# Kernel optimization log

Measured on AMD Instinct MI355X. Metric: run time of the kernel, lower is better.

## Reference

```python
import jax, jax.numpy as jnp
import numpy as np

LN_EPS = 1e-5


def sage_conv(x_src, h_dst, src, dst, num_dst, W_self, W_neigh, b):
    # DGL SAGEConv, aggregator_type='mean':
    #   h_neigh[i] = mean_{(j->i) in E} x_src[j]
    #   out = h_dst @ W_self^T + h_neigh @ W_neigh^T + b
    msg = x_src[src]  # [E, F] neighbor gather (irregular access)
    agg = jax.ops.segment_sum(msg, dst, num_segments=num_dst)  # [num_dst, F]
    deg = jax.ops.segment_sum(jnp.ones((src.shape[0],), x_src.dtype), dst,
                              num_segments=num_dst)
    h_neigh = agg / jnp.maximum(deg, 1.0)[:, None]
    return h_dst @ W_self.T + h_neigh @ W_neigh.T + b


def setup_inputs() -> dict:
    key = jax.random.key(0)
    ks = jax.random.split(key, 12)
    N0, N1, N2 = 100000, 20000, 4000
    E1, E2 = 400000, 80000
    F_IN, F_H, F_OUT = 128, 256, 64
    x = jax.random.normal(ks[0], (N0, F_IN), dtype=jnp.float32)
    # layer-1 MFG edges (src -> dst); dst nodes are the prefix x[:N1]
    src1 = jax.random.randint(ks[1], (E1,), 0, N0)
    dst1 = jax.random.randint(ks[2], (E1,), 0, N1)
    # layer-2 MFG edges over the N1 layer-1 outputs
    src2 = jax.random.randint(ks[3], (E2,), 0, N1)
    dst2 = jax.random.randint(ks[4], (E2,), 0, N2)
    s_in = 1.0 / np.sqrt(F_IN)
    s_h = 1.0 / np.sqrt(F_H)
    W_self1 = jax.random.uniform(ks[5], (F_H, F_IN), jnp.float32, -s_in, s_in)
    W_neigh1 = jax.random.uniform(ks[6], (F_H, F_IN), jnp.float32, -s_in, s_in)
    b1 = jnp.zeros((F_H,), jnp.float32)
    W_self2 = jax.random.uniform(ks[7], (F_OUT, F_H), jnp.float32, -s_h, s_h)
    W_neigh2 = jax.random.uniform(ks[8], (F_OUT, F_H), jnp.float32, -s_h, s_h)
    b2 = jnp.zeros((F_OUT,), jnp.float32)
    return {"x": x, "W_self1": W_self1, "W_neigh1": W_neigh1, "b1": b1,
            "W_self2": W_self2, "W_neigh2": W_neigh2, "b2": b2,
            "src1": src1, "dst1": dst1, "src2": src2, "dst2": dst2,
            "num_dst1": N1, "num_dst2": N2, "num_bits": 0, "num_grad_bits": 0}


def reference(x, W_self1, W_neigh1, b1, W_self2, W_neigh2, b2,
              src1, dst1, src2, dst2, num_dst1, num_dst2,
              num_bits, num_grad_bits):
    # num_bits / num_grad_bits == 0 -> full precision (quantization is identity)
    h_dst = x[:num_dst1]
    h = sage_conv(x, h_dst, src1, dst1, num_dst1, W_self1, W_neigh1, b1)
    h = jax.nn.relu(h)
    # F.layer_norm(h, h.shape): normalize over the ENTIRE tensor, no affine
    mu = jnp.mean(h)
    var = jnp.mean(jnp.square(h - mu))
    h = (h - mu) / jnp.sqrt(var + LN_EPS)
    # dropout in eval mode: identity (deterministic reference)
    h2_dst = h[:num_dst2]
    return sage_conv(h, h2_dst, src2, dst2, num_dst2, W_self2, W_neigh2, b2)
```

## Files before the change

kernel.cpp:

```cpp
#include <hip/hip_runtime.h>

#define LN_EPS 1e-5f
#define CAP 128

typedef __attribute__((ext_vector_type(8))) short short8v;
typedef __attribute__((ext_vector_type(4))) float f32x4;

__device__ __forceinline__ unsigned short f2bf(float f) {
  union { float f; unsigned u; } v; v.f = f;
  unsigned r = v.u + 0x7FFFu + ((v.u >> 16) & 1u);
  return (unsigned short)(r >> 16);
}
__device__ __forceinline__ float bf2f(unsigned short b) {
  union { unsigned u; float f; } v; v.u = ((unsigned)b) << 16;
  return v.f;
}
__device__ __forceinline__ float lo16(unsigned v) { return bf2f((unsigned short)(v & 0xffff)); }
__device__ __forceinline__ float hi16(unsigned v) { return bf2f((unsigned short)(v >> 16)); }
__device__ __forceinline__ unsigned pack2(float lo, float hi) {
  return ((unsigned)f2bf(hi) << 16) | (unsigned)f2bf(lo);
}


__global__ __launch_bounds__(256) void k_prep(
    int* __restrict__ cntz, int nz4,
    const float* __restrict__ x, unsigned short* __restrict__ xbf, int n4x,
    const float* __restrict__ wa, unsigned short* __restrict__ oa, int na4,
    const float* __restrict__ wb, unsigned short* __restrict__ ob, int nb4,
    const float* __restrict__ wc, unsigned short* __restrict__ oc, int nc4,
    const float* __restrict__ wd, unsigned short* __restrict__ od, int nd4) {
  int i = blockIdx.x * 256 + threadIdx.x;
  if (i < nz4) { ((int4*)cntz)[i] = make_int4(0, 0, 0, 0); return; }
  i -= nz4;
  const float* src;
  unsigned short* dst;
  if (i < n4x) { src = x; dst = xbf; }
  else {
    i -= n4x;
    if (i < na4) { src = wa; dst = oa; }
    else { i -= na4;
      if (i < nb4) { src = wb; dst = ob; }
      else { i -= nb4;
        if (i < nc4) { src = wc; dst = oc; }
        else { i -= nc4;
          if (i < nd4) { src = wd; dst = od; }
          else return;
        }
      }
    }
  }
  float4 v = ((const float4*)src)[i];
  ushort4 o;
  o.x = f2bf(v.x); o.y = f2bf(v.y); o.z = f2bf(v.z); o.w = f2bf(v.w);
  ((ushort4*)dst)[i] = o;
}


__global__ void k_fill2(const int* __restrict__ s1, const int* __restrict__ d1, int E1,
                        int* __restrict__ c1, int* __restrict__ l1,
                        const int* __restrict__ s2, const int* __restrict__ d2, int E2,
                        int* __restrict__ c2, int* __restrict__ l2) {
  int e = blockIdx.x * blockDim.x + threadIdx.x;
  if (e < E1) {
    int d = d1[e];
    int p = atomicAdd(&c1[d], 1);
    if (p < CAP) l1[(size_t)d * CAP + p] = s1[e];
  } else if (e < E1 + E2) {
    int k = e - E1;
    int d = d2[k];
    int p = atomicAdd(&c2[d], 1);
    if (p < CAP) l2[(size_t)d * CAP + p] = s2[k];
  }
}


__global__ __launch_bounds__(256) void k_gather1(
    const unsigned short* __restrict__ X, const int* __restrict__ cnt,
    const int* __restrict__ sl, unsigned short* __restrict__ out, int nNodes) {
  constexpr int F = 128;
  const int d = blockIdx.x * 4 + (threadIdx.x >> 6);
  if (d >= nNodes) return;
  const int lane = threadIdx.x & 63;
  const int deg = min(cnt[d], CAP);
  const int b = d * CAP;
  float a0 = 0.f, a1 = 0.f;
  const unsigned short* Xl = X + lane * 2;

  for (int j = 0; j < deg; j += 64) {
    int idx = (j + lane < deg) ? sl[b + j + lane] : 0;
    const int n = min(64, deg - j);
    int t = 0;
    for (; t + 8 <= n; t += 8) {
      unsigned v0 = *(const unsigned*)(Xl + (size_t)__shfl(idx, t + 0) * F);
      unsigned v1 = *(const unsigned*)(Xl + (size_t)__shfl(idx, t + 1) * F);
      unsigned v2 = *(const unsigned*)(Xl + (size_t)__shfl(idx, t + 2) * F);
      unsigned v3 = *(const unsigned*)(Xl + (size_t)__shfl(idx, t + 3) * F);
      unsigned v4 = *(const unsigned*)(Xl + (size_t)__shfl(idx, t + 4) * F);
      unsigned v5 = *(const unsigned*)(Xl + (size_t)__shfl(idx, t + 5) * F);
      unsigned v6 = *(const unsigned*)(Xl + (size_t)__shfl(idx, t + 6) * F);
      unsigned v7 = *(const unsigned*)(Xl + (size_t)__shfl(idx, t + 7) * F);
      a0 += lo16(v0) + lo16(v1) + lo16(v2) + lo16(v3) +
            lo16(v4) + lo16(v5) + lo16(v6) + lo16(v7);
      a1 += hi16(v0) + hi16(v1) + hi16(v2) + hi16(v3) +
            hi16(v4) + hi16(v5) + hi16(v6) + hi16(v7);
    }
    for (; t < n; ++t) {
      unsigned v = *(const unsigned*)(Xl + (size_t)__shfl(idx, t) * F);
      a0 += lo16(v);
      a1 += hi16(v);
    }
  }

  const float sc = 1.f / fmaxf((float)deg, 1.f);
  *(unsigned*)(out + (size_t)d * F + lane * 2) = pack2(a0 * sc, a1 * sc);
}


__global__ __launch_bounds__(256) void k_gather2_fin(
    const unsigned short* __restrict__ X, const int* __restrict__ cnt,
    const int* __restrict__ sl, unsigned short* __restrict__ out, int nNodes, int nGB,
    const float* __restrict__ p1, const float* __restrict__ p2, int nPart,
    float* __restrict__ stats, float invN) {
  if ((int)blockIdx.x == nGB) {
    const int tid = threadIdx.x;
    float s1 = 0.f, s2 = 0.f;
    for (int i = tid; i < nPart; i += 256) { s1 += p1[i]; s2 += p2[i]; }
#pragma unroll
    for (int o = 32; o > 0; o >>= 1) {
      s1 += __shfl_down(s1, o);
      s2 += __shfl_down(s2, o);
    }
    __shared__ float l1[4], l2[4];
    if ((tid & 63) == 0) { l1[tid >> 6] = s1; l2[tid >> 6] = s2; }
    __syncthreads();
    if (tid == 0) {
      float t1 = l1[0] + l1[1] + l1[2] + l1[3];
      float t2 = l2[0] + l2[1] + l2[2] + l2[3];
      float mu = t1 * invN;
      float var = t2 * invN - mu * mu;
      stats[2] = mu;
      stats[3] = 1.f / sqrtf(var + LN_EPS);
    }
    return;
  }

  constexpr int F = 256;
  const int d = blockIdx.x * 4 + (threadIdx.x >> 6);
  if (d >= nNodes) return;
  const int lane = threadIdx.x & 63;
  const int deg = min(cnt[d], CAP);
  const int b = d * CAP;
  float a0 = 0.f, a1 = 0.f, a2 = 0.f, a3 = 0.f;
  const unsigned short* Xl = X + lane * 4;

  for (int j = 0; j < deg; j += 64) {
    int idx = (j + lane < deg) ? sl[b + j + lane] : 0;
    const int n = min(64, deg - j);
    int t = 0;
    for (; t + 4 <= n; t += 4) {
      uint2 v0 = *(const uint2*)(Xl + (size_t)__shfl(idx, t + 0) * F);
      uint2 v1 = *(const uint2*)(Xl + (size_t)__shfl(idx, t + 1) * F);
      uint2 v2 = *(const uint2*)(Xl + (size_t)__shfl(idx, t + 2) * F);
      uint2 v3 = *(const uint2*)(Xl + (size_t)__shfl(idx, t + 3) * F);
      a0 += lo16(v0.x) + lo16(v1.x) + lo16(v2.x) + lo16(v3.x);
      a1 += hi16(v0.x) + hi16(v1.x) + hi16(v2.x) + hi16(v3.x);
      a2 += lo16(v0.y) + lo16(v1.y) + lo16(v2.y) + lo16(v3.y);
      a3 += hi16(v0.y) + hi16(v1.y) + hi16(v2.y) + hi16(v3.y);
    }
    for (; t < n; ++t) {
      uint2 v = *(const uint2*)(Xl + (size_t)__shfl(idx, t) * F);
      a0 += lo16(v.x);
      a1 += hi16(v.x);
      a2 += lo16(v.y);
      a3 += hi16(v.y);
    }
  }

  const float sc = 1.f / fmaxf((float)deg, 1.f);
  uint2 v;
  v.x = pack2(a0 * sc, a1 * sc);
  v.y = pack2(a2 * sc, a3 * sc);
  *(uint2*)(out + (size_t)d * F + lane * 4) = v;
}


__global__ __launch_bounds__(256) void k_gemm1(
    const unsigned short* __restrict__ A0, const unsigned short* __restrict__ A1,
    const unsigned short* __restrict__ B0, const unsigned short* __restrict__ B1,
    const float* __restrict__ bias, unsigned short* __restrict__ C, int M,
    float* __restrict__ part1, float* __restrict__ part2) {
  constexpr int K = 128, N = 256;
  const int lane = threadIdx.x & 63;
  const int wv = threadIdx.x >> 6;
  const int r16 = lane & 15, hi = lane >> 4;
  const int n0 = blockIdx.x * 32;
  const int m0 = blockIdx.y * 64 + wv * 16;
  int arow = m0 + r16;
  if (arow >= M) arow = M - 1;
  const int koff = hi * 8;

  short8v bf[2][4][2];
#pragma unroll
  for (int s = 0; s < 2; ++s) {
    const unsigned short* B = s ? B1 : B0;
#pragma unroll
    for (int j = 0; j < 2; ++j) {
      const unsigned short* bp = B + (size_t)(n0 + j * 16 + r16) * K + koff;
#pragma unroll
      for (int t = 0; t < 4; ++t) bf[s][t][j] = *(const short8v*)(bp + t * 32);
    }
  }

  f32x4 acc[2];
  acc[0] = f32x4{0.f, 0.f, 0.f, 0.f};
  acc[1] = f32x4{0.f, 0.f, 0.f, 0.f};
#pragma unroll
  for (int s = 0; s < 2; ++s) {
    const unsigned short* ap = (s ? A1 : A0) + (size_t)arow * K + koff;
#pragma unroll
    for (int t = 0; t < 4; ++t) {
      short8v a = *(const short8v*)(ap + t * 32);
      acc[0] = __builtin_amdgcn_mfma_f32_16x16x32_bf16(a, bf[s][t][0], acc[0], 0, 0, 0);
      acc[1] = __builtin_amdgcn_mfma_f32_16x16x32_bf16(a, bf[s][t][1], acc[1], 0, 0, 0);
    }
  }

  float s1 = 0.f, s2 = 0.f;
#pragma unroll
  for (int j = 0; j < 2; ++j) {
    const int col = n0 + j * 16 + r16;
    const float bj = bias[col];
#pragma unroll
    for (int r = 0; r < 4; ++r) {
      const int m = m0 + hi * 4 + r;
      if (m < M) {
        float c = fmaxf(acc[j][r] + bj, 0.f);
        s1 += c;
        s2 += c * c;
        C[(size_t)m * N + col] = f2bf(c);
      }
    }
  }

#pragma unroll
  for (int o = 32; o > 0; o >>= 1) {
    s1 += __shfl_down(s1, o);
    s2 += __shfl_down(s2, o);
  }
  __shared__ float l1[4], l2[4];
  if (lane == 0) { l1[wv] = s1; l2[wv] = s2; }
  __syncthreads();
  if (threadIdx.x == 0) {
    const int bid = blockIdx.y * gridDim.x + blockIdx.x;
    part1[bid] = l1[0] + l1[1] + l1[2] + l1[3];
    part2[bid] = l2[0] + l2[1] + l2[2] + l2[3];
  }
}


__device__ __forceinline__ short8v affine8(short8v v, float mu, float inv) {
  short8v r;
#pragma unroll
  for (int i = 0; i < 8; ++i) {
    r[i] = (short)f2bf((bf2f((unsigned short)v[i]) - mu) * inv);
  }
  return r;
}

__global__ __launch_bounds__(256) void k_gemm2(
    const unsigned short* __restrict__ A0, const unsigned short* __restrict__ A1,
    const unsigned short* __restrict__ B0, const unsigned short* __restrict__ B1,
    const float* __restrict__ bias, float* __restrict__ C, int M,
    const float* __restrict__ stats) {
  constexpr int K = 256, N = 64;
  const int lane = threadIdx.x & 63;
  const int wv = threadIdx.x >> 6;
  const int r16 = lane & 15, hi = lane >> 4;
  const int n0 = blockIdx.x * 16;
  const int m0 = blockIdx.y * 64 + wv * 16;
  int arow = m0 + r16;
  if (arow >= M) arow = M - 1;
  const int koff = hi * 8;
  const float mu = stats[2], inv = stats[3];

  short8v bfr[2][8];
#pragma unroll
  for (int s = 0; s < 2; ++s) {
    const unsigned short* bp = (s ? B1 : B0) + (size_t)(n0 + r16) * K + koff;
#pragma unroll
    for (int t = 0; t < 8; ++t) bfr[s][t] = *(const short8v*)(bp + t * 32);
  }

  f32x4 acc = f32x4{0.f, 0.f, 0.f, 0.f};
#pragma unroll
  for (int s = 0; s < 2; ++s) {
    const unsigned short* ap = (s ? A1 : A0) + (size_t)arow * K + koff;
#pragma unroll
    for (int t = 0; t < 8; ++t) {
      short8v a = affine8(*(const short8v*)(ap + t * 32), mu, inv);
      acc = __builtin_amdgcn_mfma_f32_16x16x32_bf16(a, bfr[s][t], acc, 0, 0, 0);
    }
  }

  const int col = n0 + r16;
  const float bj = bias[col];
#pragma unroll
  for (int r = 0; r < 4; ++r) {
    const int m = m0 + hi * 4 + r;
    if (m < M) C[(size_t)m * N + col] = acc[r] + bj;
  }
}


extern "C" void kernel_launch(void* const* d_in, const int* in_sizes, int n_in,
                              void* d_out, int out_size, void* d_ws, size_t ws_size,
                              hipStream_t stream) {
  const float* x   = (const float*)d_in[0];
  const float* Ws1 = (const float*)d_in[1];
  const float* Wn1 = (const float*)d_in[2];
  const float* b1  = (const float*)d_in[3];
  const float* Ws2 = (const float*)d_in[4];
  const float* Wn2 = (const float*)d_in[5];
  const float* b2  = (const float*)d_in[6];
  const int* src1  = (const int*)d_in[7];
  const int* dst1  = (const int*)d_in[8];
  const int* src2  = (const int*)d_in[9];
  const int* dst2  = (const int*)d_in[10];

  const int E1 = in_sizes[7];
  const int E2 = in_sizes[9];
  const int N0 = 100000, N1 = 20000, N2 = 4000;
  const int FIN = 128, FH = 256, FOUT = 64;

  char* w = (char*)d_ws;
  auto alloc = [&](size_t bytes) {
    char* p = w;
    w += (bytes + 255) & ~(size_t)255;
    return p;
  };
  int* cnt1 = (int*)alloc((size_t)(N1 + N2) * 4);
  int* cnt2 = cnt1 + N1;
  int* sl1  = (int*)alloc((size_t)N1 * CAP * 4);
  int* sl2  = (int*)alloc((size_t)N2 * CAP * 4);
  unsigned short* xbf   = (unsigned short*)alloc((size_t)N0 * FIN * 2);
  unsigned short* agg1b = (unsigned short*)alloc((size_t)N1 * FIN * 2);
  unsigned short* hbf   = (unsigned short*)alloc((size_t)N1 * FH * 2);
  unsigned short* agg2b = (unsigned short*)alloc((size_t)N2 * FH * 2);
  unsigned short* w1sb  = (unsigned short*)alloc((size_t)FH * FIN * 2);
  unsigned short* w1nb  = (unsigned short*)alloc((size_t)FH * FIN * 2);
  unsigned short* w2sb  = (unsigned short*)alloc((size_t)FOUT * FH * 2);
  unsigned short* w2nb  = (unsigned short*)alloc((size_t)FOUT * FH * 2);
  const int nBlk1 = ((N1 + 63) / 64) * (FH / 32);
  float* part1 = (float*)alloc((size_t)nBlk1 * 4);
  float* part2 = (float*)alloc((size_t)nBlk1 * 4);
  float* stats = (float*)alloc(64);

  {
    const int nz4 = (N1 + N2) / 4;
    const int n4x = N0 * FIN / 4;
    const int na4 = FH * FIN / 4, nc4 = FOUT * FH / 4;
    const int total = nz4 + n4x + 2 * na4 + 2 * nc4;
    k_prep<<<(total + 255) / 256, 256, 0, stream>>>(
        cnt1, nz4, x, xbf, n4x,
        Ws1, w1sb, na4, Wn1, w1nb, na4,
        Ws2, w2sb, nc4, Wn2, w2nb, nc4);
  }

  {
    const int Et = E1 + E2;
    k_fill2<<<(Et + 255) / 256, 256, 0, stream>>>(src1, dst1, E1, cnt1, sl1,
                                                  src2, dst2, E2, cnt2, sl2);
  }

  k_gather1<<<(N1 + 3) / 4, 256, 0, stream>>>(xbf, cnt1, sl1, agg1b, N1);

  {
    dim3 g1(FH / 32, (N1 + 63) / 64);
    k_gemm1<<<g1, 256, 0, stream>>>(xbf, agg1b, w1sb, w1nb, b1, hbf, N1, part1, part2);
  }

  {
    const int nGB = (N2 + 3) / 4;
    k_gather2_fin<<<nGB + 1, 256, 0, stream>>>(hbf, cnt2, sl2, agg2b, N2, nGB,
                                               part1, part2, nBlk1, stats,
                                               1.f / ((float)N1 * (float)FH));
  }

  {
    dim3 g2(FOUT / 16, (N2 + 63) / 64);
    k_gemm2<<<g2, 256, 0, stream>>>(hbf, agg2b, w2sb, w2nb, b2, (float*)d_out, N2, stats);
  }
}
```

Before: 107.4 us.

## Fuse layer-1 gather and GEMM, gather fp32 x directly, drop x bf16 conversion

The separate layer-1 gather and GEMM kernels are merged into one kernel per 64-row tile. Each wave gathers neighbour means for 16 rows from fp32 x into shared memory, then computes all 256 output columns with MFMA. The self-term rows are converted from fp32 to bf16 in registers, so the prep kernel no longer converts all of x to bf16 and the bf16 x and aggregate buffers disappear. The cost is fewer blocks (about 313), so the gather has less parallelism, and gathered rows are fp32, which doubles bytes per neighbour row. Weight tiles are also reloaded for each of the 8 column chunks.

```diff
diff --git a/kernel.cpp b/kernel.cpp
--- a/kernel.cpp
+++ b/kernel.cpp
@@ -20,39 +20,32 @@
 __device__ __forceinline__ unsigned pack2(float lo, float hi) {
   return ((unsigned)f2bf(hi) << 16) | (unsigned)f2bf(lo);
 }
+__device__ __forceinline__ short8v cvt8(float4 a, float4 b) {
+  short8v r;
+  r[0] = (short)f2bf(a.x); r[1] = (short)f2bf(a.y);
+  r[2] = (short)f2bf(a.z); r[3] = (short)f2bf(a.w);
+  r[4] = (short)f2bf(b.x); r[5] = (short)f2bf(b.y);
+  r[6] = (short)f2bf(b.z); r[7] = (short)f2bf(b.w);
+  return r;
+}
 
 
 __global__ __launch_bounds__(256) void k_prep(
     int* __restrict__ cntz, int nz4,
-    const float* __restrict__ x, unsigned short* __restrict__ xbf, int n4x,
-    const float* __restrict__ wa, unsigned short* __restrict__ oa, int na4,
-    const float* __restrict__ wb, unsigned short* __restrict__ ob, int nb4,
-    const float* __restrict__ wc, unsigned short* __restrict__ oc, int nc4,
-    const float* __restrict__ wd, unsigned short* __restrict__ od, int nd4) {
+    const float* __restrict__ wa, unsigned short* __restrict__ oa, int na,
+    const float* __restrict__ wb, unsigned short* __restrict__ ob, int nb,
+    const float* __restrict__ wc, unsigned short* __restrict__ oc, int nc,
+    const float* __restrict__ wd, unsigned short* __restrict__ od, int nd) {
   int i = blockIdx.x * 256 + threadIdx.x;
   if (i < nz4) { ((int4*)cntz)[i] = make_int4(0, 0, 0, 0); return; }
   i -= nz4;
-  const float* src;
-  unsigned short* dst;
-  if (i < n4x) { src = x; dst = xbf; }
-  else {
-    i -= n4x;
-    if (i < na4) { src = wa; dst = oa; }
-    else { i -= na4;
-      if (i < nb4) { src = wb; dst = ob; }
-      else { i -= nb4;
-        if (i < nc4) { src = wc; dst = oc; }
-        else { i -= nc4;
-          if (i < nd4) { src = wd; dst = od; }
-          else return;
-        }
-      }
-    }
-  }
-  float4 v = ((const float4*)src)[i];
-  ushort4 o;
-  o.x = f2bf(v.x); o.y = f2bf(v.y); o.z = f2bf(v.z); o.w = f2bf(v.w);
-  ((ushort4*)dst)[i] = o;
+  if (i < na) { oa[i] = f2bf(wa[i]); return; }
+  i -= na;
+  if (i < nb) { ob[i] = f2bf(wb[i]); return; }
+  i -= nb;
+  if (i < nc) { oc[i] = f2bf(wc[i]); return; }
+  i -= nc;
+  if (i < nd) { od[i] = f2bf(wd[i]); }
 }
 
 
@@ -74,45 +67,125 @@
 }
 
 
-__global__ __launch_bounds__(256) void k_gather1(
-    const unsigned short* __restrict__ X, const int* __restrict__ cnt,
-    const int* __restrict__ sl, unsigned short* __restrict__ out, int nNodes) {
-  constexpr int F = 128;
-  const int d = blockIdx.x * 4 + (threadIdx.x >> 6);
-  if (d >= nNodes) return;
-  const int lane = threadIdx.x & 63;
-  const int deg = min(cnt[d], CAP);
-  const int b = d * CAP;
-  float a0 = 0.f, a1 = 0.f;
-  const unsigned short* Xl = X + lane * 2;
-
-  for (int j = 0; j < deg; j += 64) {
-    int idx = (j + lane < deg) ? sl[b + j + lane] : 0;
-    const int n = min(64, deg - j);
-    int t = 0;
-    for (; t + 8 <= n; t += 8) {
-      unsigned v0 = *(const unsigned*)(Xl + (size_t)__shfl(idx, t + 0) * F);
-      unsigned v1 = *(const unsigned*)(Xl + (size_t)__shfl(idx, t + 1) * F);
-      unsigned v2 = *(const unsigned*)(Xl + (size_t)__shfl(idx, t + 2) * F);
-      unsigned v3 = *(const unsigned*)(Xl + (size_t)__shfl(idx, t + 3) * F);
-      unsigned v4 = *(const unsigned*)(Xl + (size_t)__shfl(idx, t + 4) * F);
-      unsigned v5 = *(const unsigned*)(Xl + (size_t)__shfl(idx, t + 5) * F);
-      unsigned v6 = *(const unsigned*)(Xl + (size_t)__shfl(idx, t + 6) * F);
-      unsigned v7 = *(const unsigned*)(Xl + (size_t)__shfl(idx, t + 7) * F);
-      a0 += lo16(v0) + lo16(v1) + lo16(v2) + lo16(v3) +
-            lo16(v4) + lo16(v5) + lo16(v6) + lo16(v7);
-      a1 += hi16(v0) + hi16(v1) + hi16(v2) + hi16(v3) +
-            hi16(v4) + hi16(v5) + hi16(v6) + hi16(v7);
-    }
-    for (; t < n; ++t) {
-      unsigned v = *(const unsigned*)(Xl + (size_t)__shfl(idx, t) * F);
-      a0 += lo16(v);
-      a1 += hi16(v);
-    }
-  }
-
-  const float sc = 1.f / fmaxf((float)deg, 1.f);
-  *(unsigned*)(out + (size_t)d * F + lane * 2) = pack2(a0 * sc, a1 * sc);
+__global__ __launch_bounds__(256) void k_l1(
+    const float* __restrict__ X, const int* __restrict__ cnt, const int* __restrict__ sl,
+    const unsigned short* __restrict__ B0, const unsigned short* __restrict__ B1,
+    const float* __restrict__ bias, unsigned short* __restrict__ H, int M,
+    float* __restrict__ part1, float* __restrict__ part2) {
+  constexpr int K = 128, N = 256;
+  __shared__ unsigned aggS[64][68];
+  const int tid = threadIdx.x;
+  const int lane = tid & 63;
+  const int wv = tid >> 6;
+  const int mBase = blockIdx.x * 64;
+
+  for (int i = 0; i < 16; ++i) {
+    const int d = mBase + wv * 16 + i;
+    if (d >= M) break;
+    const int deg = min(cnt[d], CAP);
+    const int b = d * CAP;
+    float a0 = 0.f, a1 = 0.f;
+    const float* Xl = X + lane * 2;
+    for (int j = 0; j < deg; j += 64) {
+      int idx = (j + lane < deg) ? sl[b + j + lane] : 0;
+      const int n = min(64, deg - j);
+      int t = 0;
+      for (; t + 8 <= n; t += 8) {
+        float2 v0 = *(const float2*)(Xl + (size_t)__shfl(idx, t + 0) * K);
+        float2 v1 = *(const float2*)(Xl + (size_t)__shfl(idx, t + 1) * K);
+        float2 v2 = *(const float2*)(Xl + (size_t)__shfl(idx, t + 2) * K);
+        float2 v3 = *(const float2*)(Xl + (size_t)__shfl(idx, t + 3) * K);
+        float2 v4 = *(const float2*)(Xl + (size_t)__shfl(idx, t + 4) * K);
+        float2 v5 = *(const float2*)(Xl + (size_t)__shfl(idx, t + 5) * K);
+        float2 v6 = *(const float2*)(Xl + (size_t)__shfl(idx, t + 6) * K);
+        float2 v7 = *(const float2*)(Xl + (size_t)__shfl(idx, t + 7) * K);
+        a0 += v0.x + v1.x + v2.x + v3.x + v4.x + v5.x + v6.x + v7.x;
+        a1 += v0.y + v1.y + v2.y + v3.y + v4.y + v5.y + v6.y + v7.y;
+      }
+      for (; t < n; ++t) {
+        float2 v = *(const float2*)(Xl + (size_t)__shfl(idx, t) * K);
+        a0 += v.x;
+        a1 += v.y;
+      }
+    }
+    const float sc = 1.f / fmaxf((float)deg, 1.f);
+    aggS[wv * 16 + i][lane] = pack2(a0 * sc, a1 * sc);
+  }
+  __syncthreads();
+
+  const int r16 = lane & 15, hi4 = lane >> 4;
+  const int koff = hi4 * 8;
+  const int m0 = mBase + wv * 16;
+  int arow = m0 + r16;
+  if (arow >= M) arow = M - 1;
+  const int lr = arow - mBase;
+
+  short8v a0f[4], a1f[4];
+  {
+    const float* ap = X + (size_t)arow * K + koff;
+#pragma unroll
+    for (int t = 0; t < 4; ++t) {
+      a0f[t] = cvt8(*(const float4*)(ap + t * 32), *(const float4*)(ap + t * 32 + 4));
+      uint4 u = *(const uint4*)&aggS[lr][hi4 * 4 + t * 16];
+      union { uint4 u; short8v s; } cast;
+      cast.u = u;
+      a1f[t] = cast.s;
+    }
+  }
+
+  float s1 = 0.f, s2 = 0.f;
+  for (int j0 = 0; j0 < 8; ++j0) {
+    const int n0 = j0 * 32;
+    short8v bf[2][4][2];
+#pragma unroll
+    for (int s = 0; s < 2; ++s) {
+      const unsigned short* B = s ? B1 : B0;
+#pragma unroll
+      for (int j = 0; j < 2; ++j) {
+        const unsigned short* bp = B + (size_t)(n0 + j * 16 + r16) * K + koff;
+#pragma unroll
+        for (int t = 0; t < 4; ++t) bf[s][t][j] = *(const short8v*)(bp + t * 32);
+      }
+    }
+
+    f32x4 acc[2];
+    acc[0] = f32x4{0.f, 0.f, 0.f, 0.f};
+    acc[1] = f32x4{0.f, 0.f, 0.f, 0.f};
+#pragma unroll
+    for (int t = 0; t < 4; ++t) {
+      acc[0] = __builtin_amdgcn_mfma_f32_16x16x32_bf16(a0f[t], bf[0][t][0], acc[0], 0, 0, 0);
+      acc[1] = __builtin_amdgcn_mfma_f32_16x16x32_bf16(a0f[t], bf[0][t][1], acc[1], 0, 0, 0);
+      acc[0] = __builtin_amdgcn_mfma_f32_16x16x32_bf16(a1f[t], bf[1][t][0], acc[0], 0, 0, 0);
+      acc[1] = __builtin_amdgcn_mfma_f32_16x16x32_bf16(a1f[t], bf[1][t][1], acc[1], 0, 0, 0);
+    }
+
+#pragma unroll
+    for (int j = 0; j < 2; ++j) {
+      const int col = n0 + j * 16 + r16;
+      const float bj = bias[col];
+#pragma unroll
+      for (int r = 0; r < 4; ++r) {
+        const int m = m0 + hi4 * 4 + r;
+        if (m < M) {
+          float c = fmaxf(acc[j][r] + bj, 0.f);
+          s1 += c;
+          s2 += c * c;
+          H[(size_t)m * N + col] = f2bf(c);
+        }
+      }
+    }
+  }
+
+#pragma unroll
+  for (int o = 32; o > 0; o >>= 1) {
+    s1 += __shfl_down(s1, o);
+    s2 += __shfl_down(s2, o);
+  }
+  if (lane == 0) {
+    const int bid = blockIdx.x * 4 + wv;
+    part1[bid] = s1;
+    part2[bid] = s2;
+  }
 }
 
 
@@ -181,80 +254,6 @@
   v.x = pack2(a0 * sc, a1 * sc);
   v.y = pack2(a2 * sc, a3 * sc);
   *(uint2*)(out + (size_t)d * F + lane * 4) = v;
-}
-
-
-__global__ __launch_bounds__(256) void k_gemm1(
-    const unsigned short* __restrict__ A0, const unsigned short* __restrict__ A1,
-    const unsigned short* __restrict__ B0, const unsigned short* __restrict__ B1,
-    const float* __restrict__ bias, unsigned short* __restrict__ C, int M,
-    float* __restrict__ part1, float* __restrict__ part2) {
-  constexpr int K = 128, N = 256;
-  const int lane = threadIdx.x & 63;
-  const int wv = threadIdx.x >> 6;
-  const int r16 = lane & 15, hi = lane >> 4;
-  const int n0 = blockIdx.x * 32;
-  const int m0 = blockIdx.y * 64 + wv * 16;
-  int arow = m0 + r16;
-  if (arow >= M) arow = M - 1;
-  const int koff = hi * 8;
-
-  short8v bf[2][4][2];
-#pragma unroll
-  for (int s = 0; s < 2; ++s) {
-    const unsigned short* B = s ? B1 : B0;
-#pragma unroll
-    for (int j = 0; j < 2; ++j) {
-      const unsigned short* bp = B + (size_t)(n0 + j * 16 + r16) * K + koff;
-#pragma unroll
-      for (int t = 0; t < 4; ++t) bf[s][t][j] = *(const short8v*)(bp + t * 32);
-    }
-  }
-
-  f32x4 acc[2];
-  acc[0] = f32x4{0.f, 0.f, 0.f, 0.f};
-  acc[1] = f32x4{0.f, 0.f, 0.f, 0.f};
-#pragma unroll
-  for (int s = 0; s < 2; ++s) {
-    const unsigned short* ap = (s ? A1 : A0) + (size_t)arow * K + koff;
-#pragma unroll
-    for (int t = 0; t < 4; ++t) {
-      short8v a = *(const short8v*)(ap + t * 32);
-      acc[0] = __builtin_amdgcn_mfma_f32_16x16x32_bf16(a, bf[s][t][0], acc[0], 0, 0, 0);
-      acc[1] = __builtin_amdgcn_mfma_f32_16x16x32_bf16(a, bf[s][t][1], acc[1], 0, 0, 0);
-    }
-  }
-
-  float s1 = 0.f, s2 = 0.f;
-#pragma unroll
-  for (int j = 0; j < 2; ++j) {
-    const int col = n0 + j * 16 + r16;
-    const float bj = bias[col];
-#pragma unroll
-    for (int r = 0; r < 4; ++r) {
-      const int m = m0 + hi * 4 + r;
-      if (m < M) {
-        float c = fmaxf(acc[j][r] + bj, 0.f);
-        s1 += c;
-        s2 += c * c;
-        C[(size_t)m * N + col] = f2bf(c);
-      }
-    }
-  }
-
-#pragma unroll
-  for (int o = 32; o > 0; o >>= 1) {
-    s1 += __shfl_down(s1, o);
-    s2 += __shfl_down(s2, o);
-  }
-  __shared__ float l1[4], l2[4];
-  if (lane == 0) { l1[wv] = s1; l2[wv] = s2; }
-  __syncthreads();
-  if (threadIdx.x == 0) {
-    const int bid = blockIdx.y * gridDim.x + blockIdx.x;
-    part1[bid] = l1[0] + l1[1] + l1[2] + l1[3];
-    part2[bid] = l2[0] + l2[1] + l2[2] + l2[3];
-  }
 }
 
 
@@ -329,7 +328,7 @@
 
   const int E1 = in_sizes[7];
   const int E2 = in_sizes[9];
-  const int N0 = 100000, N1 = 20000, N2 = 4000;
+  const int N1 = 20000, N2 = 4000;
   const int FIN = 128, FH = 256, FOUT = 64;
 
   char* w = (char*)d_ws;
@@ -342,28 +341,24 @@
   int* cnt2 = cnt1 + N1;
   int* sl1  = (int*)alloc((size_t)N1 * CAP * 4);
   int* sl2  = (int*)alloc((size_t)N2 * CAP * 4);
-  unsigned short* xbf   = (unsigned short*)alloc((size_t)N0 * FIN * 2);
-  unsigned short* agg1b = (unsigned short*)alloc((size_t)N1 * FIN * 2);
   unsigned short* hbf   = (unsigned short*)alloc((size_t)N1 * FH * 2);
   unsigned short* agg2b = (unsigned short*)alloc((size_t)N2 * FH * 2);
   unsigned short* w1sb  = (unsigned short*)alloc((size_t)FH * FIN * 2);
   unsigned short* w1nb  = (unsigned short*)alloc((size_t)FH * FIN * 2);
   unsigned short* w2sb  = (unsigned short*)alloc((size_t)FOUT * FH * 2);
   unsigned short* w2nb  = (unsigned short*)alloc((size_t)FOUT * FH * 2);
-  const int nBlk1 = ((N1 + 63) / 64) * (FH / 32);
-  float* part1 = (float*)alloc((size_t)nBlk1 * 4);
-  float* part2 = (float*)alloc((size_t)nBlk1 * 4);
+  const int mTiles = (N1 + 63) / 64;
+  const int nPart = mTiles * 4;
+  float* part1 = (float*)alloc((size_t)nPart * 4);
+  float* part2 = (float*)alloc((size_t)nPart * 4);
   float* stats = (float*)alloc(64);
 
   {
     const int nz4 = (N1 + N2) / 4;
-    const int n4x = N0 * FIN / 4;
-    const int na4 = FH * FIN / 4, nc4 = FOUT * FH / 4;
-    const int total = nz4 + n4x + 2 * na4 + 2 * nc4;
+    const int na = FH * FIN, nc = FOUT * FH;
+    const int total = nz4 + 2 * na + 2 * nc;
     k_prep<<<(total + 255) / 256, 256, 0, stream>>>(
-        cnt1, nz4, x, xbf, n4x,
-        Ws1, w1sb, na4, Wn1, w1nb, na4,
-        Ws2, w2sb, nc4, Wn2, w2nb, nc4);
+        cnt1, nz4, Ws1, w1sb, na, Wn1, w1nb, na, Ws2, w2sb, nc, Wn2, w2nb, nc);
   }
 
   {
@@ -372,17 +367,12 @@
                                                   src2, dst2, E2, cnt2, sl2);
   }
 
-  k_gather1<<<(N1 + 3) / 4, 256, 0, stream>>>(xbf, cnt1, sl1, agg1b, N1);
-
-  {
-    dim3 g1(FH / 32, (N1 + 63) / 64);
-    k_gemm1<<<g1, 256, 0, stream>>>(xbf, agg1b, w1sb, w1nb, b1, hbf, N1, part1, part2);
-  }
+  k_l1<<<mTiles, 256, 0, stream>>>(x, cnt1, sl1, w1sb, w1nb, b1, hbf, N1, part1, part2);
 
   {
     const int nGB = (N2 + 3) / 4;
     k_gather2_fin<<<nGB + 1, 256, 0, stream>>>(hbf, cnt2, sl2, agg2b, N2, nGB,
-                                               part1, part2, nBlk1, stats,
+                                               part1, part2, nPart, stats,
                                                1.f / ((float)N1 * (float)FH));
   }
 
```

After: 143.6 us. +33.8%, slower.
